# Kernel optimization log

Hardware: AMD Instinct MI355X
Metric: run time of the kernel (lower is better)

Reference implementation:

```python
import jax, jax.numpy as jnp
import numpy as np

V, D, H, C = 100000, 300, 16, 5
B, T = 256, 128


def setup_inputs() -> dict:
    key = jax.random.key(0)
    ks = jax.random.split(key, 8)
    s = 1.0 / np.sqrt(H).astype(np.float32)  # PyTorch LSTM/Linear init range
    x = jax.random.randint(ks[0], (B, T), 0, V)
    emb = jax.random.normal(ks[1], (V, D), jnp.float32) * 0.02
    W_ih = jax.random.uniform(ks[2], (4 * H, D), jnp.float32, -s, s)
    W_hh = jax.random.uniform(ks[3], (4 * H, H), jnp.float32, -s, s)
    b_ih = jax.random.uniform(ks[4], (4 * H,), jnp.float32, -s, s)
    b_hh = jax.random.uniform(ks[5], (4 * H,), jnp.float32, -s, s)
    W_out = jax.random.uniform(ks[6], (C, H), jnp.float32, -s, s)
    b_out = jax.random.uniform(ks[7], (C,), jnp.float32, -s, s)
    return dict(x=x, emb=emb, W_ih=W_ih, W_hh=W_hh, b_ih=b_ih, b_hh=b_hh,
                W_out=W_out, b_out=b_out)


def reference(x, emb, W_ih, W_hh, b_ih, b_hh, W_out, b_out):
    h_dim = W_hh.shape[1]
    xe = emb[x]  # [B,T,D] embedding lookup
    # Precompute input contribution to all 4 gates for all timesteps (one big GEMM).
    xg = jnp.einsum('btd,gd->btg', xe, W_ih) + b_ih + b_hh  # [B,T,4H]
    xg = jnp.transpose(xg, (1, 0, 2))  # [T,B,4H] time-major for scan
    b = x.shape[0]
    h0 = jnp.zeros((b, h_dim), xg.dtype)
    c0 = jnp.zeros((b, h_dim), xg.dtype)

    def step(carry, g_t):
        h, c = carry
        g = g_t + h @ W_hh.T  # [B,4H]
        i, f, gg, o = jnp.split(g, 4, axis=-1)  # PyTorch gate order: i,f,g,o
        i = jax.nn.sigmoid(i)
        f = jax.nn.sigmoid(f)
        gg = jnp.tanh(gg)
        o = jax.nn.sigmoid(o)
        c = f * c + i * gg
        h = o * jnp.tanh(c)
        return (h, c), h

    _, hs = jax.lax.scan(step, (h0, c0), xg)  # hs: [T,B,H]
    hs = jnp.transpose(hs, (1, 0, 2))  # [B,T,H]
    return hs @ W_out.T + b_out  # [B,T,C]
```

## Files before the change

### kernel.cpp

```cpp
#include <hip/hip_runtime.h>
#include <cstdint>

#define BB 256
#define TT 128
#define DD 300
#define HH 16
#define GG 64
#define CC 5
#define NKS 10
#define XSTR 132
#define L2E 1.4426950408889634f

typedef __attribute__((ext_vector_type(8))) short short8;
typedef __attribute__((ext_vector_type(4))) float float4v;

static __device__ inline unsigned short f2bf(float f) {
  unsigned u = __float_as_uint(f);
  return (unsigned short)((u + 0x7FFFu + ((u >> 16) & 1u)) >> 16);
}
static __device__ inline float bf2f(unsigned short h) {
  return __uint_as_float(((unsigned)h) << 16);
}

__global__ __launch_bounds__(256, 1) void lstm_fused_kernel(
    const int* __restrict__ x, const float* __restrict__ emb,
    const float* __restrict__ W_ih, const float* __restrict__ W_hh,
    const float* __restrict__ b_ih, const float* __restrict__ b_hh,
    const float* __restrict__ W_out, const float* __restrict__ b_out,
    float* __restrict__ out) {

  __shared__ unsigned short Bh[NKS * 4 * 64 * 8];
  __shared__ unsigned short Bl[NKS * 4 * 64 * 8];
  __shared__ float uni[19264];

  float* rawW = uni;
  float* xgsT = uni;
  float* hsm  = uni + GG * XSTR;

  const int t = threadIdx.x;
  const int b = blockIdx.x;
  const int w = t >> 6;
  const int lane = t & 63;
  const int m = lane & 15, quad = lane >> 4;

  {
    const float4* __restrict__ src = (const float4*)W_ih;
    float4* dst = (float4*)rawW;
#pragma unroll
    for (int i = 0; i < 18; i++) dst[t + 256 * i] = src[t + 256 * i];
    if (t < 192) dst[t + 256 * 18] = src[t + 256 * 18];
  }
  __syncthreads();

  for (int si = 0; si < 10; si++) {
    const int s = w * 10 + si;
    const int ks = s >> 2, nt = s & 3;
    const int c = nt * 16 + m;
    const int k0 = ks * 32 + quad * 8;
    float4 z4 = {0.f, 0.f, 0.f, 0.f};
    float4 w0 = z4, w1 = z4;
    if (k0 + 4 <= DD) w0 = *(const float4*)&rawW[c * DD + k0];
    if (k0 + 8 <= DD) w1 = *(const float4*)&rawW[c * DD + k0 + 4];
    float wf[8] = {w0.x, w0.y, w0.z, w0.w, w1.x, w1.y, w1.z, w1.w};
    short8 h8, l8;
#pragma unroll
    for (int jj = 0; jj < 8; jj++) {
      unsigned short hb = f2bf(wf[jj]);
      h8[jj] = (short)hb;
      l8[jj] = (short)f2bf(wf[jj] - bf2f(hb));
    }
    const int base = (s * 64 + lane) * 8;
    *(short8*)&Bh[base] = h8;
    *(short8*)&Bl[base] = l8;
  }
  __syncthreads();

  {
    const int xr0 = x[b * TT + w * 32 + m];
    const int xr1 = x[b * TT + w * 32 + 16 + m];
    const float* __restrict__ arow0 = emb + (size_t)xr0 * DD + quad * 8;
    const float* __restrict__ arow1 = emb + (size_t)xr1 * DD + quad * 8;

    float4v acc[2][4];
#pragma unroll
    for (int mt = 0; mt < 2; mt++)
#pragma unroll
      for (int nt = 0; nt < 4; nt++) acc[mt][nt] = (float4v){0.f, 0.f, 0.f, 0.f};

    float4 pre[2][2][2];
    auto issue = [&](int ks) {
      if (ks < 9) {
        const int p = ks & 1;
        pre[p][0][0] = *(const float4*)(arow0 + ks * 32);
        pre[p][0][1] = *(const float4*)(arow0 + ks * 32 + 4);
        pre[p][1][0] = *(const float4*)(arow1 + ks * 32);
        pre[p][1][1] = *(const float4*)(arow1 + ks * 32 + 4);
      } else if (ks == 9) {
        const int k0t = 288 + quad * 8;
        float4 z4 = {0.f, 0.f, 0.f, 0.f};
        pre[1][0][0] = (k0t + 4 <= DD) ? *(const float4*)(arow0 + 288) : z4;
        pre[1][0][1] = (k0t + 8 <= DD) ? *(const float4*)(arow0 + 292) : z4;
        pre[1][1][0] = (k0t + 4 <= DD) ? *(const float4*)(arow1 + 288) : z4;
        pre[1][1][1] = (k0t + 8 <= DD) ? *(const float4*)(arow1 + 292) : z4;
      }
    };
    issue(0);
    issue(1);

#pragma unroll
    for (int ks = 0; ks < NKS; ks++) {
      const int p = ks & 1;
      short8 ah[2], al[2];
#pragma unroll
      for (int mt = 0; mt < 2; mt++) {
        float af[8] = {pre[p][mt][0].x, pre[p][mt][0].y, pre[p][mt][0].z,
                       pre[p][mt][0].w, pre[p][mt][1].x, pre[p][mt][1].y,
                       pre[p][mt][1].z, pre[p][mt][1].w};
#pragma unroll
        for (int jj = 0; jj < 8; jj++) {
          unsigned short hb = f2bf(af[jj]);
          ah[mt][jj] = (short)hb;
          al[mt][jj] = (short)f2bf(af[jj] - bf2f(hb));
        }
      }
      issue(ks + 2);

#pragma unroll
      for (int nt = 0; nt < 4; nt++) {
        const int base = ((ks * 4 + nt) * 64 + lane) * 8;
        short8 bh = *(const short8*)&Bh[base];
        short8 bl = *(const short8*)&Bl[base];
#pragma unroll
        for (int mt = 0; mt < 2; mt++) {
          acc[mt][nt] = __builtin_amdgcn_mfma_f32_16x16x32_bf16(ah[mt], bh, acc[mt][nt], 0, 0, 0);
          acc[mt][nt] = __builtin_amdgcn_mfma_f32_16x16x32_bf16(al[mt], bh, acc[mt][nt], 0, 0, 0);
          acc[mt][nt] = __builtin_amdgcn_mfma_f32_16x16x32_bf16(ah[mt], bl, acc[mt][nt], 0, 0, 0);
        }
      }
    }

#pragma unroll
    for (int nt = 0; nt < 4; nt++) {
      const int col = nt * 16 + m;
      const float scale = (nt == 2) ? (-2.0f * L2E) : (-L2E);
      const float bias = b_ih[col] + b_hh[col];
#pragma unroll
      for (int mt = 0; mt < 2; mt++) {
#pragma unroll
        for (int reg = 0; reg < 4; reg++) {
          const int ts = w * 32 + mt * 16 + quad * 4 + reg;
          xgsT[col * XSTR + ts] = (acc[mt][nt][reg] + bias) * scale;
        }
      }
    }
  }
  __syncthreads();

  if (t < 64) {
    const int k = lane >> 2;
    const int g = lane & 3;
    const int j = g * 16 + k;
    const float wscale = (g == 2) ? (-2.0f * L2E) : (-L2E);
    const float Aa = (g == 2) ? (-4.0f * L2E) : 1.0f;
    const float Ba = (g == 2) ? (2.0f * L2E) : 0.0f;

    float wh[16];
#pragma unroll
    for (int kk = 0; kk < 16; kk++) wh[kk] = W_hh[j * HH + kk] * wscale;

    float cs = 0.0f;
    float hu[16];
#pragma unroll
    for (int kk = 0; kk < 16; kk++) hu[kk] = 0.0f;

    const float* __restrict__ gptr = &xgsT[j * XSTR];
    float4 gA = *(const float4*)gptr;
    float4 gB = *(const float4*)(gptr + 4);

    for (int ch = 0; ch < 32; ch++) {
      float4 gC = (ch < 30) ? *(const float4*)(gptr + 4 * (ch + 2)) : gA;
      float ga[4] = {gA.x, gA.y, gA.z, gA.w};
#pragma unroll
      for (int s4 = 0; s4 < 4; s4++) {
        const int ts = ch * 4 + s4;
        float a0 = fmaf(hu[0], wh[0], ga[s4]);
        a0 = fmaf(hu[1], wh[1], a0);
        a0 = fmaf(hu[2], wh[2], a0);
        a0 = fmaf(hu[3], wh[3], a0);
        float a1 = hu[4] * wh[4];
        a1 = fmaf(hu[5], wh[5], a1);
        a1 = fmaf(hu[6], wh[6], a1);
        a1 = fmaf(hu[7], wh[7], a1);
        float a2 = hu[8] * wh[8];
        a2 = fmaf(hu[9], wh[9], a2);
        a2 = fmaf(hu[10], wh[10], a2);
        a2 = fmaf(hu[11], wh[11], a2);
        float a3 = hu[12] * wh[12];
        a3 = fmaf(hu[13], wh[13], a3);
        a3 = fmaf(hu[14], wh[14], a3);
        a3 = fmaf(hu[15], wh[15], a3);
        float gv = (a0 + a1) + (a2 + a3);

        float e = __builtin_amdgcn_exp2f(gv);
        float s = __builtin_amdgcn_rcpf(1.0f + e);
        float act = fmaf(Aa, s, Ba);

        int ai = __float_as_int(act);
        float iv = __int_as_float(__builtin_amdgcn_update_dpp(ai, ai, 0x00, 0xF, 0xF, true));
        float fv = __int_as_float(__builtin_amdgcn_update_dpp(ai, ai, 0x55, 0xF, 0xF, true));
        float gs = __int_as_float(__builtin_amdgcn_update_dpp(ai, ai, 0xAA, 0xF, 0xF, true));
        float ov = __int_as_float(__builtin_amdgcn_update_dpp(ai, ai, 0xFF, 0xF, 0xF, true));

        cs = fmaf(fv, cs, iv * gs);
        float e2 = __builtin_amdgcn_exp2f(cs);
        float tc = fmaf(2.0f, __builtin_amdgcn_rcpf(1.0f + e2), -1.0f);
        float hnew = ov * tc;

        hsm[ts * GG + lane] = hnew;

#pragma unroll
        for (int kk = 0; kk < 16; kk++)
          hu[kk] = __uint_as_float(
              __builtin_amdgcn_readlane(__float_as_uint(hnew), 4 * kk));
      }
      gA = gB; gB = gC;
    }
  }
  __syncthreads();

  float* outb = out + (size_t)b * TT * CC;
  for (int idx = t; idx < TT * CC; idx += 256) {
    int tt2 = idx / CC;
    int cc = idx - tt2 * CC;
    const float* wr = W_out + cc * HH;
    float accv = b_out[cc];
#pragma unroll
    for (int kk = 0; kk < 16; kk++)
      accv = fmaf(hsm[tt2 * GG + 4 * kk], wr[kk], accv);
    outb[idx] = accv;
  }
}

extern "C" void kernel_launch(void* const* d_in, const int* in_sizes, int n_in,
                              void* d_out, int out_size, void* d_ws, size_t ws_size,
                              hipStream_t stream) {
  const int*   x     = (const int*)d_in[0];
  const float* emb   = (const float*)d_in[1];
  const float* W_ih  = (const float*)d_in[2];
  const float* W_hh  = (const float*)d_in[3];
  const float* b_ih  = (const float*)d_in[4];
  const float* b_hh  = (const float*)d_in[5];
  const float* W_out = (const float*)d_in[6];
  const float* b_out = (const float*)d_in[7];
  float* out = (float*)d_out;

  lstm_fused_kernel<<<BB, 256, 0, stream>>>(x, emb, W_ih, W_hh, b_ih, b_hh,
                                            W_out, b_out, out);
}
```

Baseline: 196.8 us.

## Split fused LSTM into weight-prep, input GEMM, and recurrence kernels

Replaces the single fused per-batch kernel with three launches. The first builds the split-bf16 W_ih fragments once, the second runs the embedding/input-projection GEMM across 512 blocks and writes gate pre-activations to workspace, and the third runs the serial recurrence reading those from global memory. This is meant to stop every block from redundantly converting W_ih and to spread the GEMM over more parallel blocks. In exchange it adds two extra launches and an 8 MB global round-trip for the gate pre-activations. The recurrence now streams its inputs from global/L2 instead of LDS.

```diff
diff --git a/kernel.cpp b/kernel.cpp
--- a/kernel.cpp
+++ b/kernel.cpp
@@ -8,7 +8,7 @@
 #define GG 64
 #define CC 5
 #define NKS 10
-#define XSTR 132
+#define HSTR 68
 #define L2E 1.4426950408889634f
 
 typedef __attribute__((ext_vector_type(8))) short short8;
@@ -22,139 +22,120 @@
   return __uint_as_float(((unsigned)h) << 16);
 }
 
-__global__ __launch_bounds__(256, 1) void lstm_fused_kernel(
+
+__global__ __launch_bounds__(64) void frag_build_kernel(
+    const float* __restrict__ W_ih,
+    unsigned short* __restrict__ Bh_g, unsigned short* __restrict__ Bl_g) {
+  const int s = blockIdx.x;
+  const int lane = threadIdx.x;
+  const int m = lane & 15, quad = lane >> 4;
+  const int ks = s >> 2, nt = s & 3;
+  const int c = nt * 16 + m;
+  const int k0 = ks * 32 + quad * 8;
+  float4 z4 = {0.f, 0.f, 0.f, 0.f};
+  float4 w0 = z4, w1 = z4;
+  if (k0 + 4 <= DD) w0 = *(const float4*)&W_ih[c * DD + k0];
+  if (k0 + 8 <= DD) w1 = *(const float4*)&W_ih[c * DD + k0 + 4];
+  float wf[8] = {w0.x, w0.y, w0.z, w0.w, w1.x, w1.y, w1.z, w1.w};
+  short8 h8, l8;
+#pragma unroll
+  for (int jj = 0; jj < 8; jj++) {
+    unsigned short hb = f2bf(wf[jj]);
+    h8[jj] = (short)hb;
+    l8[jj] = (short)f2bf(wf[jj] - bf2f(hb));
+  }
+  const int base = (s * 64 + lane) * 8;
+  *(short8*)&Bh_g[base] = h8;
+  *(short8*)&Bl_g[base] = l8;
+}
+
+__global__ __launch_bounds__(256, 2) void lstm_gemm_kernel(
     const int* __restrict__ x, const float* __restrict__ emb,
-    const float* __restrict__ W_ih, const float* __restrict__ W_hh,
+    const unsigned short* __restrict__ Bh_g,
+    const unsigned short* __restrict__ Bl_g,
     const float* __restrict__ b_ih, const float* __restrict__ b_hh,
-    const float* __restrict__ W_out, const float* __restrict__ b_out,
-    float* __restrict__ out) {
-
-  __shared__ unsigned short Bh[NKS * 4 * 64 * 8];
-  __shared__ unsigned short Bl[NKS * 4 * 64 * 8];
-  __shared__ float uni[19264];
-
-  float* rawW = uni;
-  float* xgsT = uni;
-  float* hsm  = uni + GG * XSTR;
-
+    float* __restrict__ xgT) {
   const int t = threadIdx.x;
-  const int b = blockIdx.x;
+  const int gb = blockIdx.x;
+  const int b = gb >> 1;
   const int w = t >> 6;
   const int lane = t & 63;
   const int m = lane & 15, quad = lane >> 4;
-
-  {
-    const float4* __restrict__ src = (const float4*)W_ih;
-    float4* dst = (float4*)rawW;
-#pragma unroll
-    for (int i = 0; i < 18; i++) dst[t + 256 * i] = src[t + 256 * i];
-    if (t < 192) dst[t + 256 * 18] = src[t + 256 * 18];
-  }
-  __syncthreads();
-
-  for (int si = 0; si < 10; si++) {
-    const int s = w * 10 + si;
-    const int ks = s >> 2, nt = s & 3;
-    const int c = nt * 16 + m;
-    const int k0 = ks * 32 + quad * 8;
-    float4 z4 = {0.f, 0.f, 0.f, 0.f};
-    float4 w0 = z4, w1 = z4;
-    if (k0 + 4 <= DD) w0 = *(const float4*)&rawW[c * DD + k0];
-    if (k0 + 8 <= DD) w1 = *(const float4*)&rawW[c * DD + k0 + 4];
-    float wf[8] = {w0.x, w0.y, w0.z, w0.w, w1.x, w1.y, w1.z, w1.w};
-    short8 h8, l8;
-#pragma unroll
-    for (int jj = 0; jj < 8; jj++) {
-      unsigned short hb = f2bf(wf[jj]);
-      h8[jj] = (short)hb;
-      l8[jj] = (short)f2bf(wf[jj] - bf2f(hb));
-    }
-    const int base = (s * 64 + lane) * 8;
-    *(short8*)&Bh[base] = h8;
-    *(short8*)&Bl[base] = l8;
-  }
-  __syncthreads();
-
-  {
-    const int xr0 = x[b * TT + w * 32 + m];
-    const int xr1 = x[b * TT + w * 32 + 16 + m];
-    const float* __restrict__ arow0 = emb + (size_t)xr0 * DD + quad * 8;
-    const float* __restrict__ arow1 = emb + (size_t)xr1 * DD + quad * 8;
-
-    float4v acc[2][4];
-#pragma unroll
-    for (int mt = 0; mt < 2; mt++)
-#pragma unroll
-      for (int nt = 0; nt < 4; nt++) acc[mt][nt] = (float4v){0.f, 0.f, 0.f, 0.f};
-
-    float4 pre[2][2][2];
-    auto issue = [&](int ks) {
-      if (ks < 9) {
-        const int p = ks & 1;
-        pre[p][0][0] = *(const float4*)(arow0 + ks * 32);
-        pre[p][0][1] = *(const float4*)(arow0 + ks * 32 + 4);
-        pre[p][1][0] = *(const float4*)(arow1 + ks * 32);
-        pre[p][1][1] = *(const float4*)(arow1 + ks * 32 + 4);
-      } else if (ks == 9) {
-        const int k0t = 288 + quad * 8;
-        float4 z4 = {0.f, 0.f, 0.f, 0.f};
-        pre[1][0][0] = (k0t + 4 <= DD) ? *(const float4*)(arow0 + 288) : z4;
-        pre[1][0][1] = (k0t + 8 <= DD) ? *(const float4*)(arow0 + 292) : z4;
-        pre[1][1][0] = (k0t + 4 <= DD) ? *(const float4*)(arow1 + 288) : z4;
-        pre[1][1][1] = (k0t + 8 <= DD) ? *(const float4*)(arow1 + 292) : z4;
+  const int tbase = (gb & 1) * 64 + w * 16;
+
+  const int xr = x[b * TT + tbase + m];
+  const float* __restrict__ arow = emb + (size_t)xr * DD + quad * 8;
+
+  float4v acc[4];
+#pragma unroll
+  for (int nt = 0; nt < 4; nt++) acc[nt] = (float4v){0.f, 0.f, 0.f, 0.f};
+
+  float4 pre[2][2];
+  auto issue = [&](int ks) {
+    if (ks < 9) {
+      const int p = ks & 1;
+      pre[p][0] = *(const float4*)(arow + ks * 32);
+      pre[p][1] = *(const float4*)(arow + ks * 32 + 4);
+    } else if (ks == 9) {
+      const int k0t = 288 + quad * 8;
+      float4 z4 = {0.f, 0.f, 0.f, 0.f};
+      pre[1][0] = (k0t + 4 <= DD) ? *(const float4*)(arow + 288) : z4;
+      pre[1][1] = (k0t + 8 <= DD) ? *(const float4*)(arow + 292) : z4;
+    }
+  };
+  issue(0);
+  issue(1);
+
+#pragma unroll
+  for (int ks = 0; ks < NKS; ks++) {
+    const int p = ks & 1;
+    short8 ah, al;
+    {
+      float af[8] = {pre[p][0].x, pre[p][0].y, pre[p][0].z, pre[p][0].w,
+                     pre[p][1].x, pre[p][1].y, pre[p][1].z, pre[p][1].w};
+#pragma unroll
+      for (int jj = 0; jj < 8; jj++) {
+        unsigned short hb = f2bf(af[jj]);
+        ah[jj] = (short)hb;
+        al[jj] = (short)f2bf(af[jj] - bf2f(hb));
       }
-    };
-    issue(0);
-    issue(1);
-
-#pragma unroll
-    for (int ks = 0; ks < NKS; ks++) {
-      const int p = ks & 1;
-      short8 ah[2], al[2];
-#pragma unroll
-      for (int mt = 0; mt < 2; mt++) {
-        float af[8] = {pre[p][mt][0].x, pre[p][mt][0].y, pre[p][mt][0].z,
-                       pre[p][mt][0].w, pre[p][mt][1].x, pre[p][mt][1].y,
-                       pre[p][mt][1].z, pre[p][mt][1].w};
-#pragma unroll
-        for (int jj = 0; jj < 8; jj++) {
-          unsigned short hb = f2bf(af[jj]);
-          ah[mt][jj] = (short)hb;
-          al[mt][jj] = (short)f2bf(af[jj] - bf2f(hb));
-        }
-      }
-      issue(ks + 2);
-
-#pragma unroll
-      for (int nt = 0; nt < 4; nt++) {
-        const int base = ((ks * 4 + nt) * 64 + lane) * 8;
-        short8 bh = *(const short8*)&Bh[base];
-        short8 bl = *(const short8*)&Bl[base];
-#pragma unroll
-        for (int mt = 0; mt < 2; mt++) {
-          acc[mt][nt] = __builtin_amdgcn_mfma_f32_16x16x32_bf16(ah[mt], bh, acc[mt][nt], 0, 0, 0);
-          acc[mt][nt] = __builtin_amdgcn_mfma_f32_16x16x32_bf16(al[mt], bh, acc[mt][nt], 0, 0, 0);
-          acc[mt][nt] = __builtin_amdgcn_mfma_f32_16x16x32_bf16(ah[mt], bl, acc[mt][nt], 0, 0, 0);
-        }
-      }
-    }
+    }
+    issue(ks + 2);
 
 #pragma unroll
     for (int nt = 0; nt < 4; nt++) {
-      const int col = nt * 16 + m;
-      const float scale = (nt == 2) ? (-2.0f * L2E) : (-L2E);
-      const float bias = b_ih[col] + b_hh[col];
-#pragma unroll
-      for (int mt = 0; mt < 2; mt++) {
-#pragma unroll
-        for (int reg = 0; reg < 4; reg++) {
-          const int ts = w * 32 + mt * 16 + quad * 4 + reg;
-          xgsT[col * XSTR + ts] = (acc[mt][nt][reg] + bias) * scale;
-        }
-      }
-    }
-  }
-  __syncthreads();
+      const int base = ((ks * 4 + nt) * 64 + lane) * 8;
+      short8 bh = *(const short8*)&Bh_g[base];
+      short8 bl = *(const short8*)&Bl_g[base];
+      acc[nt] = __builtin_amdgcn_mfma_f32_16x16x32_bf16(ah, bh, acc[nt], 0, 0, 0);
+      acc[nt] = __builtin_amdgcn_mfma_f32_16x16x32_bf16(al, bh, acc[nt], 0, 0, 0);
+      acc[nt] = __builtin_amdgcn_mfma_f32_16x16x32_bf16(ah, bl, acc[nt], 0, 0, 0);
+    }
+  }
+
+#pragma unroll
+  for (int nt = 0; nt < 4; nt++) {
+    const int col = nt * 16 + m;
+    const float scale = (nt == 2) ? (-2.0f * L2E) : (-L2E);
+    const float bias = b_ih[col] + b_hh[col];
+    float4 v;
+    v.x = (acc[nt][0] + bias) * scale;
+    v.y = (acc[nt][1] + bias) * scale;
+    v.z = (acc[nt][2] + bias) * scale;
+    v.w = (acc[nt][3] + bias) * scale;
+    *(float4*)&xgT[(size_t)b * (TT * GG) + col * TT + tbase + quad * 4] = v;
+  }
+}
+
+__global__ __launch_bounds__(256, 1) void lstm_rec_kernel(
+    const float* __restrict__ xg, const float* __restrict__ W_hh,
+    const float* __restrict__ W_out, const float* __restrict__ b_out,
+    float* __restrict__ out) {
+  __shared__ float hsm[TT * HSTR];
+
+  const int t = threadIdx.x;
+  const int b = blockIdx.x;
+  const int lane = t & 63;
 
   if (t < 64) {
     const int k = lane >> 2;
@@ -173,7 +154,7 @@
 #pragma unroll
     for (int kk = 0; kk < 16; kk++) hu[kk] = 0.0f;
 
-    const float* __restrict__ gptr = &xgsT[j * XSTR];
+    const float* __restrict__ gptr = xg + (size_t)b * (TT * GG) + j * TT;
     float4 gA = *(const float4*)gptr;
     float4 gB = *(const float4*)(gptr + 4);
 
@@ -216,14 +197,15 @@
         float tc = fmaf(2.0f, __builtin_amdgcn_rcpf(1.0f + e2), -1.0f);
         float hnew = ov * tc;
 
-        hsm[ts * GG + lane] = hnew;
+        hsm[ts * HSTR + lane] = hnew;
 
 #pragma unroll
         for (int kk = 0; kk < 16; kk++)
           hu[kk] = __uint_as_float(
               __builtin_amdgcn_readlane(__float_as_uint(hnew), 4 * kk));
       }
-      gA = gB; gB = gC;
+      gA = gB;
+      gB = gC;
     }
   }
   __syncthreads();
@@ -236,7 +218,7 @@
     float accv = b_out[cc];
 #pragma unroll
     for (int kk = 0; kk < 16; kk++)
-      accv = fmaf(hsm[tt2 * GG + 4 * kk], wr[kk], accv);
+      accv = fmaf(hsm[tt2 * HSTR + 4 * kk], wr[kk], accv);
     outb[idx] = accv;
   }
 }
@@ -254,6 +236,12 @@
   const float* b_out = (const float*)d_in[7];
   float* out = (float*)d_out;
 
-  lstm_fused_kernel<<<BB, 256, 0, stream>>>(x, emb, W_ih, W_hh, b_ih, b_hh,
-                                            W_out, b_out, out);
-}
+  float* xgT = (float*)d_ws;
+  unsigned short* Bh_g =
+      (unsigned short*)((char*)d_ws + (size_t)BB * TT * GG * 4);
+  unsigned short* Bl_g = Bh_g + NKS * 4 * 64 * 8;
+
+  frag_build_kernel<<<40, 64, 0, stream>>>(W_ih, Bh_g, Bl_g);
+  lstm_gemm_kernel<<<512, 256, 0, stream>>>(x, emb, Bh_g, Bl_g, b_ih, b_hh, xgT);
+  lstm_rec_kernel<<<BB, 256, 0, stream>>>(xgT, W_hh, W_out, b_out, out);
+}
```

After: 202.9 us. 3.1% more time.
